# Kernel tuning notes

Measured on AMD Instinct MI355X. Metric: run time of the kernel, lower is better.

Reference implementation:

```python
import jax, jax.numpy as jnp
import numpy as np

B, S, DIM, EXTRA, NK, NH, NL = 16, 256, 41, 1, 128, 4, 3
ND = DIM + EXTRA  # 42 channels after appending the Time2Vec extra channel


def _lin(key, fin, fout):
    kw, kb = jax.random.split(key)
    w = jax.random.normal(kw, (fin, fout), jnp.float32) / np.float32(np.sqrt(fin))
    b = jax.random.normal(kb, (fout,), jnp.float32) * 0.01
    return w, b


def _stack(key, fin, fout):
    ws, bs = zip(*[_lin(k, fin, fout) for k in jax.random.split(key, NL)])
    return jnp.stack(ws), jnp.stack(bs)


def setup_inputs():
    key = jax.random.key(0)
    ks = jax.random.split(key, 32)
    inp = {}
    inp['context_x'] = jnp.sort(jax.random.uniform(ks[0], (B, S), jnp.float32), axis=1)
    inp['value'] = jax.random.normal(ks[1], (B, S, DIM), jnp.float32)
    mask = (jax.random.uniform(ks[2], (B, S, DIM)) < 0.23).astype(jnp.float32)
    inp['mask'] = mask
    inp['target_value'] = jax.random.normal(ks[3], (B, S, DIM), jnp.float32)
    inp['target_mask'] = mask * (jax.random.uniform(ks[4], (B, S, DIM)) < 0.3).astype(jnp.float32)
    inp['t2v_w0'] = jax.random.normal(ks[5], (1,), jnp.float32)
    inp['t2v_b0'] = jax.random.normal(ks[6], (1,), jnp.float32)
    inp['edge_w'], inp['edge_b'] = _lin(ks[7], 2, NK)
    inp['chan_w'], inp['chan_b'] = _lin(ks[8], ND, NK)
    inp['time_w'], inp['time_b'] = _lin(ks[9], 1, NK)
    base = 10
    for pre, dk in (('ct', 2 * NK), ('tc', 2 * NK), ('ca', NK)):
        inp[pre + '_wq'], inp[pre + '_bq'] = _stack(ks[base], NK, NK); base += 1
        inp[pre + '_wk'], inp[pre + '_bk'] = _stack(ks[base], dk, NK); base += 1
        inp[pre + '_wv'], inp[pre + '_bv'] = _stack(ks[base], dk, NK); base += 1
        inp[pre + '_wo'], inp[pre + '_bo'] = _stack(ks[base], NK, NK); base += 1
    inp['en_w'], inp['en_b'] = _stack(ks[base], 3 * NK, NK); base += 1
    inp['out_w'], inp['out_b'] = _lin(ks[base], 3 * NK, 1)
    return inp


def _mab2(Q, K, wq, bq, wk, bk, wv, bv, wo, bo, mask):
    # GraFITi MAB2: fc_q/fc_k/fc_v -> dim_out, multihead attn, O = Q + A@V, then O += relu(fc_o(O))
    q = Q @ wq + bq
    k = K @ wk + bk
    v = K @ wv + bv
    b, nq, d = q.shape
    dh = d // NH
    qh = q.reshape(b, nq, NH, dh)
    kh = k.reshape(b, -1, NH, dh)
    vh = v.reshape(b, -1, NH, dh)
    att = jnp.einsum('bqhd,bkhd->bhqk', qh, kh) / np.float32(np.sqrt(d))
    if mask is not None:
        att = jnp.where(mask[:, None] == 0, jnp.float32(-1e10), att)
    A = jax.nn.softmax(att, axis=-1)
    o = (qh + jnp.einsum('bhqk,bkhd->bqhd', A, vh)).reshape(b, nq, d)
    return o + jax.nn.relu(o @ wo + bo)


def _forward(context_x, value, mask, target_value, target_mask, t2v_w0, t2v_b0,
             edge_w, edge_b, chan_w, chan_b, time_w, time_b,
             ct_wq, ct_bq, ct_wk, ct_bk, ct_wv, ct_bv, ct_wo, ct_bo,
             tc_wq, tc_bq, tc_wk, tc_bk, tc_wv, tc_bv, tc_wo, tc_bo,
             en_w, en_b,
             ca_wq, ca_bq, ca_wk, ca_bk, ca_wv, ca_bv, ca_wo, ca_bo,
             out_w, out_b):
    te = (t2v_w0 * context_x + t2v_b0)[:, :, None]  # Time2Vec linear channel [B,S,1]
    value_f = jnp.concatenate([value, te], -1)  # [B,S,ND]
    mask_f = jnp.concatenate([mask, jnp.ones((B, S, EXTRA), jnp.float32)], -1)
    tval_f = jnp.concatenate([target_value, te], -1)
    tmask_f = jnp.concatenate([target_mask, jnp.zeros((B, S, EXTRA), jnp.float32)], -1)
    # ragged compaction: observed entries first, zero-padded to the batch max count
    full_len = int(np.asarray(jnp.max(jnp.sum(mask_f, axis=(1, 2)))))
    order = jnp.argsort(-mask_f.reshape(B, -1), axis=1, stable=True)[:, :full_len]
    take = lambda x: jnp.take_along_axis(x.reshape(B, -1), order, axis=1)
    mk_ = take(mask_f)  # [B,L]: ones then zero padding
    U_val = take(value_f) * mk_
    target_U_ = take(tval_f) * mk_
    target_mask_ = take(tmask_f) * mk_
    mki = mk_.astype(jnp.int32)
    T_inds_ = take(jnp.broadcast_to(jnp.arange(S, dtype=jnp.int32)[None, :, None], (B, S, ND))) * mki
    C_inds_ = take(jnp.broadcast_to(jnp.arange(ND, dtype=jnp.int32)[None, None, :], (B, S, ND))) * mki
    C_mask = (C_inds_[:, None, :] == jnp.arange(ND)[None, :, None]).astype(jnp.float32) * mk_[:, None, :]
    T_mask = (T_inds_[:, None, :] == jnp.arange(S)[None, :, None]).astype(jnp.float32) * mk_[:, None, :]
    U_ind = 1.0 - mk_ + target_mask_
    U = jax.nn.relu(jnp.stack([U_val, U_ind], -1) @ edge_w + edge_b) * mk_[:, :, None]  # [B,L,NK]
    T_ = jnp.sin(context_x[:, :, None] @ time_w + time_b)  # [B,S,NK]
    # one_hot(arange(ND)) @ chan_w == chan_w
    C_ = jnp.broadcast_to(jax.nn.relu(chan_w + chan_b)[None], (B, ND, NK))
    gT = lambda x, idx: jnp.take_along_axis(x, jnp.broadcast_to(idx[:, :, None], (B, full_len, NK)), axis=1)
    for i in range(NL):
        k_t = gT(T_, T_inds_)
        C2 = _mab2(C_, jnp.concatenate([k_t, U], -1), ct_wq[i], ct_bq[i], ct_wk[i], ct_bk[i], ct_wv[i], ct_bv[i], ct_wo[i], ct_bo[i], C_mask)
        k_c = gT(C_, C_inds_)
        T2 = _mab2(T_, jnp.concatenate([k_c, U], -1), tc_wq[i], tc_bq[i], tc_wk[i], tc_bk[i], tc_wv[i], tc_bv[i], tc_wo[i], tc_bo[i], T_mask)
        U = jax.nn.relu(U + jnp.concatenate([U, k_t, k_c], -1) @ en_w[i] + en_b[i]) * mk_[:, :, None]
        C_ = _mab2(C2, C2, ca_wq[i], ca_bq[i], ca_wk[i], ca_bk[i], ca_wv[i], ca_bv[i], ca_wo[i], ca_bo[i], None)
        T_ = T2
    k_t = gT(T_, T_inds_)
    k_c = gT(C_, C_inds_)
    output = jnp.concatenate([U, k_t, k_c], -1) @ out_w + out_b  # [B,L,1]
    return output, target_U_, target_mask_


def reference(context_x, value, mask, target_value, target_mask, t2v_w0, t2v_b0, edge_w, edge_b, chan_w, chan_b, time_w, time_b, ct_wq, ct_bq, ct_wk, ct_bk, ct_wv, ct_bv, ct_wo, ct_bo, tc_wq, tc_bq, tc_wk, tc_bk, tc_wv, tc_bv, tc_wo, tc_bo, en_w, en_b, ca_wq, ca_bq, ca_wk, ca_bk, ca_wv, ca_bv, ca_wo, ca_bo, out_w, out_b):
    return _forward(context_x, value, mask, target_value, target_mask, t2v_w0, t2v_b0, edge_w, edge_b, chan_w, chan_b, time_w, time_b, ct_wq, ct_bq, ct_wk, ct_bk, ct_wv, ct_bv, ct_wo, ct_bo, tc_wq, tc_bq, tc_wk, tc_bk, tc_wv, tc_bv, tc_wo, tc_bo, en_w, en_b, ca_wq, ca_bq, ca_wk, ca_bk, ca_wv, ca_bv, ca_wo, ca_bo, out_w, out_b)
```

## Files before the change

### kernel.cpp

```cpp
#include <hip/hip_runtime.h>
#include <math.h>

#define NB   16
#define SS   256
#define DIMV 41
#define NDV  42
#define NKD  128
#define NHD  4
#define DH   32
#define NLAY 3
#define TOT  (SS*NDV)
#define NCH  42

typedef __attribute__((ext_vector_type(8))) short short8;
typedef __attribute__((ext_vector_type(4))) float floatx4;

__device__ __forceinline__ short f2bf(float x) {
    unsigned u = __float_as_uint(x);
    u += 0x7fff + ((u >> 16) & 1);
    return (short)(u >> 16);
}
__device__ __forceinline__ float bfs2f(short s) {
    return __uint_as_float(((unsigned)(unsigned short)s) << 16);
}
__device__ __forceinline__ float bf2f(unsigned s) {
    return __uint_as_float(s << 16);
}

struct Seg { const short* ptr; const int* ind; int ns; };

__device__ __forceinline__ const short* seg_row(const Seg s, int gm, int Lb) {
    if (s.ind) {
        int b = gm / Lb;
        int id = s.ind[gm]; if (id < 0) id = 0;
        return s.ptr + ((size_t)b * s.ns + (size_t)id) * NKD;
    }
    return s.ptr + (size_t)gm * NKD;
}


__device__ __forceinline__ void compactA_body(int bx, const float* __restrict__ maskp,
                                              int* __restrict__ chunkcnt)
{
    const int b = bx / NCH, ch = bx % NCH;
    const int tid = threadIdx.x;
    const int idx = ch * 256 + tid;
    const int s = idx / NDV, c = idx % NDV;
    float m = (c < DIMV) ? maskp[((size_t)b*SS + s)*DIMV + c] : 1.0f;
    int x = (m != 0.0f) ? 1 : 0;
    #pragma unroll
    for (int off = 32; off; off >>= 1) x += __shfl_down(x, off);
    __shared__ int ws4[4];
    if ((tid & 63) == 0) ws4[tid >> 6] = x;
    __syncthreads();
    if (tid == 0) chunkcnt[bx] = ws4[0] + ws4[1] + ws4[2] + ws4[3];
}

__device__ __forceinline__ void zero_body(int bx, int* __restrict__ lo_t,
                                          int* __restrict__ hi_t)
{
    int i = bx*256 + threadIdx.x;
    if (i < NB*SS) { lo_t[i] = 0; hi_t[i] = 0; }
}

__device__ __forceinline__ void initT_body(int bx, const float* __restrict__ cx,
                                           const float* __restrict__ tw,
                                           const float* __restrict__ tb,
                                           short* __restrict__ T)
{
    int i = bx * 256 + threadIdx.x;
    if (i >= NB*SS*16) return;
    int row = i >> 4;
    int k = (i & 15) << 3;
    float t = cx[row];
    short8 r;
    #pragma unroll
    for (int j = 0; j < 8; j++) r[j] = f2bf(sinf(t*tw[k+j] + tb[k+j]));
    *(short8*)(T + (size_t)row*NKD + k) = r;
}

__device__ __forceinline__ void initC_body(int bx, const float* __restrict__ cw,
                                           const float* __restrict__ cb,
                                           short* __restrict__ C)
{
    int i = bx * 256 + threadIdx.x;
    if (i >= NB*NDV*16) return;
    int row = i >> 4;
    int c = row % NDV;
    int k = (i & 15) << 3;
    short8 r;
    #pragma unroll
    for (int j = 0; j < 8; j++) r[j] = f2bf(fmaxf(cw[(size_t)c*NKD + k+j] + cb[k+j], 0.f));
    *(short8*)(C + (size_t)row*NKD + k) = r;
}

template<int Kg>
__device__ __forceinline__ void prep1(const float* __restrict__ src,
                                      short* __restrict__ dst, int rel)
{
    const int per = Kg*128;
    int i = rel / per; int r2 = rel - i*per;
    int n = r2 / Kg;   int k = r2 - n*Kg;
    dst[rel] = f2bf(src[(size_t)i*per + (size_t)k*128 + n]);
}

#define W_TOTAL 933888
__device__ __forceinline__ void prepw_body(int bx,
    const float* ctq, const float* ctk, const float* ctv, const float* cto,
    const float* tcq, const float* tck, const float* tcv, const float* tco,
    const float* caq, const float* cak, const float* cav, const float* cao,
    const float* enw, short* __restrict__ arena)
{
    int idx = bx*256 + threadIdx.x;
    if (idx >= W_TOTAL) return;
    if      (idx < 49152 ) prep1<128>(ctq, arena + 0,      idx - 0);
    else if (idx < 147456) prep1<256>(ctk, arena + 49152,  idx - 49152);
    else if (idx < 245760) prep1<256>(ctv, arena + 147456, idx - 147456);
    else if (idx < 294912) prep1<128>(cto, arena + 245760, idx - 245760);
    else if (idx < 344064) prep1<128>(tcq, arena + 294912, idx - 294912);
    else if (idx < 442368) prep1<256>(tck, arena + 344064, idx - 344064);
    else if (idx < 540672) prep1<256>(tcv, arena + 442368, idx - 442368);
    else if (idx < 589824) prep1<128>(tco, arena + 540672, idx - 540672);
    else if (idx < 638976) prep1<128>(caq, arena + 589824, idx - 589824);
    else if (idx < 688128) prep1<128>(cak, arena + 638976, idx - 638976);
    else if (idx < 737280) prep1<128>(cav, arena + 688128, idx - 688128);
    else if (idx < 786432) prep1<128>(cao, arena + 737280, idx - 737280);
    else                   prep1<384>(enw, arena + 786432, idx - 786432);
}

__device__ __forceinline__ void trange_body(int bx, const int* __restrict__ tind,
                                            int* __restrict__ lo_t,
                                            int* __restrict__ hi_t, int L)
{
    int p = bx*256 + threadIdx.x;
    if (p >= NB*L) return;
    int b = p / L, l = p - b*L;
    int t = tind[p];
    if (t < 0) return;
    int tp = (l > 0) ? tind[p-1] : -999;
    int tn = (l+1 < L) ? tind[p+1] : -999;
    if (tp != t) lo_t[b*SS + t] = l;
    if (tn != t) hi_t[b*SS + t] = l+1;
}

__device__ __forceinline__ void cperm_body(int b, const int* __restrict__ cind,
                                           int* __restrict__ invp,
                                           int* __restrict__ clo,
                                           int* __restrict__ chi, int L)
{
    __shared__ int hist[NDV];
    __shared__ int base[NDV];
    __shared__ int padc, cntsh;
    const int tid = threadIdx.x;
    if (tid < NDV) hist[tid] = 0;
    if (tid == 0) padc = 0;
    __syncthreads();
    for (int l = tid; l < L; l += 256) {
        int c = cind[(size_t)b*L + l];
        if (c >= 0) atomicAdd(&hist[c], 1);
    }
    __syncthreads();
    if (tid == 0) {
        int run = 0;
        for (int c = 0; c < NDV; c++) {
            base[c] = run; clo[b*NDV + c] = run;
            run += hist[c]; chi[b*NDV + c] = run;
        }
        cntsh = run;
    }
    __syncthreads();
    if (tid < NDV) hist[tid] = 0;
    __syncthreads();
    const int cnt = cntsh;
    for (int l = tid; l < L; l += 256) {
        int c = cind[(size_t)b*L + l];
        int pos;
        if (c >= 0) pos = base[c] + atomicAdd(&hist[c], 1);
        else        pos = cnt + atomicAdd(&padc, 1);
        invp[(size_t)b*L + l] = b*L + pos;
    }
}

__device__ __forceinline__ void initU_body(int bx, const float* __restrict__ uval,
                                           const float* __restrict__ uind,
                                           const float* __restrict__ mkb,
                                           const float* __restrict__ ew,
                                           const float* __restrict__ eb,
                                           short* __restrict__ U, int BL)
{
    int i = bx * 256 + threadIdx.x;
    if (i >= BL*16) return;
    int row = i >> 4;
    int k = (i & 15) << 3;
    float uv = uval[row], ui = uind[row], m = mkb[row];
    short8 r;
    #pragma unroll
    for (int j = 0; j < 8; j++)
        r[j] = f2bf(fmaxf(uv*ew[k+j] + ui*ew[NKD+k+j] + eb[k+j], 0.f) * m);
    *(short8*)(U + (size_t)row*NKD + k) = r;
}

template<int NSEG, int MODE>
__device__ __forceinline__ void mgemm_body(char* smem, int bx,
           Seg s0, Seg s1, Seg s2, const short* __restrict__ Wt,
           const float* __restrict__ bias, short* __restrict__ D,
           int M, int Lb, const float* __restrict__ mkp)
{
    short (*As)[40] = (short (*)[40])smem;
    short (*Bs)[40] = (short (*)[40])(smem + 10240);
    const int bm = bx * 128;
    const int tid = threadIdx.x;
    const int wv = tid >> 6;
    const int lane = tid & 63;
    const int quad = lane >> 4;
    const int l16 = lane & 15;
    const int K = NSEG * 128;
    floatx4 acc[2][8];
    #pragma unroll
    for (int i = 0; i < 2; i++)
        #pragma unroll
        for (int j = 0; j < 8; j++) acc[i][j] = (floatx4){0.f,0.f,0.f,0.f};

    const int arow = tid >> 1;
    const int acol = (tid & 1) * 16;
    int gmc = bm + arow; if (gmc > M-1) gmc = M-1;
    const short* rowp0 = seg_row(s0, gmc, Lb);
    const short* rowp1 = (NSEG > 1) ? seg_row(s1, gmc, Lb) : nullptr;
    const short* rowp2 = (NSEG > 2) ? seg_row(s2, gmc, Lb) : nullptr;

    for (int k0 = 0; k0 < K; k0 += 32) {
        {
            const short* rp;
            if (NSEG == 1) rp = rowp0;
            else if (NSEG == 2) rp = (k0 < 128) ? rowp0 : rowp1;
            else rp = (k0 < 128) ? rowp0 : ((k0 < 256) ? rowp1 : rowp2);
            const int ks = k0 & 127;
            const short* src = rp + ks + acol;
            *(short8*)&As[arow][acol]   = *(const short8*)(src);
            *(short8*)&As[arow][acol+8] = *(const short8*)(src+8);
        }
        {
            const short* src = Wt + (size_t)arow*K + k0 + acol;
            *(short8*)&Bs[arow][acol]   = *(const short8*)(src);
            *(short8*)&Bs[arow][acol+8] = *(const short8*)(src+8);
        }
        __syncthreads();
        short8 af0 = *(short8*)&As[wv*32 + l16][quad*8];
        short8 af1 = *(short8*)&As[wv*32 + 16 + l16][quad*8];
        #pragma unroll
        for (int nf = 0; nf < 8; nf++) {
            short8 bf = *(short8*)&Bs[nf*16 + l16][quad*8];
            acc[0][nf] = __builtin_amdgcn_mfma_f32_16x16x32_bf16(af0, bf, acc[0][nf], 0, 0, 0);
            acc[1][nf] = __builtin_amdgcn_mfma_f32_16x16x32_bf16(af1, bf, acc[1][nf], 0, 0, 0);
        }
        __syncthreads();
    }
    #pragma unroll
    for (int mf = 0; mf < 2; mf++) {
        #pragma unroll
        for (int r = 0; r < 4; r++) {
            int gm = bm + wv*32 + mf*16 + quad*4 + r;
            if (gm < M) {
                float mk = (MODE == 3) ? mkp[gm] : 0.f;
                const short* res = (MODE == 2 || MODE == 3) ? seg_row(s0, gm, Lb) : nullptr;
                #pragma unroll
                for (int nf = 0; nf < 8; nf++) {
                    int gn = nf*16 + l16;
                    float val = acc[mf][nf][r] + bias[gn];
                    if (MODE == 2) val = bfs2f(res[gn]) + fmaxf(val, 0.f);
                    else if (MODE == 3) val = fmaxf(bfs2f(res[gn]) + val, 0.f) * mk;
                    D[(size_t)gm*NKD + gn] = f2bf(val);
                }
            }
        }
    }
}

template<int NSEG, bool HASQ>
__device__ __forceinline__ void mgemm_kv_body(char* smem, int bx,
              Seg s0, Seg s1,
              const short* __restrict__ Wk, const float* __restrict__ bk,
              const short* __restrict__ Wv, const float* __restrict__ bv,
              const short* __restrict__ Wq, const float* __restrict__ bq,
              short* __restrict__ Qd,
              unsigned* __restrict__ KV, int M, int Lb, const int* __restrict__ rmap)
{
    short (*As)[40] = (short (*)[40])smem;
    short (*Bk_)[40] = (short (*)[40])(smem + 5120);
    short (*Bv_)[40] = (short (*)[40])(smem + 15360);
    short (*Bq_)[40] = (short (*)[40])(smem + 25600);
    const int bm = bx * 64;
    const int tid = threadIdx.x;
    const int wv = tid >> 6;
    const int lane = tid & 63;
    const int quad = lane >> 4;
    const int l16 = lane & 15;
    const int K = NSEG * 128;
    floatx4 acck[8], accv[8], accq[8];
    #pragma unroll
    for (int j = 0; j < 8; j++) {
        acck[j] = (floatx4){0.f,0.f,0.f,0.f};
        accv[j] = (floatx4){0.f,0.f,0.f,0.f};
        if (HASQ) accq[j] = (floatx4){0.f,0.f,0.f,0.f};
    }

    const int arow = tid >> 2;
    const int acol = (tid & 3) * 8;
    const int brow = tid >> 1;
    const int bcol = (tid & 1) * 16;
    int gmc = bm + arow; if (gmc > M-1) gmc = M-1;
    const short* rowp0 = seg_row(s0, gmc, Lb);
    const short* rowp1 = (NSEG > 1) ? seg_row(s1, gmc, Lb) : nullptr;

    for (int k0 = 0; k0 < K; k0 += 32) {
        {
            const short* rp = (NSEG == 1) ? rowp0 : ((k0 < 128) ? rowp0 : rowp1);
            const int ks = k0 & 127;
            *(short8*)&As[arow][acol] = *(const short8*)(rp + ks + acol);
        }
        {
            const short* sk = Wk + (size_t)brow*K + k0 + bcol;
            *(short8*)&Bk_[brow][bcol]   = *(const short8*)(sk);
            *(short8*)&Bk_[brow][bcol+8] = *(const short8*)(sk+8);
            const short* sv = Wv + (size_t)brow*K + k0 + bcol;
            *(short8*)&Bv_[brow][bcol]   = *(const short8*)(sv);
            *(short8*)&Bv_[brow][bcol+8] = *(const short8*)(sv+8);
            if (HASQ) {
                const short* sq = Wq + (size_t)brow*K + k0 + bcol;
                *(short8*)&Bq_[brow][bcol]   = *(const short8*)(sq);
                *(short8*)&Bq_[brow][bcol+8] = *(const short8*)(sq+8);
            }
        }
        __syncthreads();
        short8 af = *(short8*)&As[wv*16 + l16][quad*8];
        #pragma unroll
        for (int nf = 0; nf < 8; nf++) {
            short8 bfk = *(short8*)&Bk_[nf*16 + l16][quad*8];
            acck[nf] = __builtin_amdgcn_mfma_f32_16x16x32_bf16(af, bfk, acck[nf], 0, 0, 0);
            short8 bfv = *(short8*)&Bv_[nf*16 + l16][quad*8];
            accv[nf] = __builtin_amdgcn_mfma_f32_16x16x32_bf16(af, bfv, accv[nf], 0, 0, 0);
            if (HASQ) {
                short8 bfq = *(short8*)&Bq_[nf*16 + l16][quad*8];
                accq[nf] = __builtin_amdgcn_mfma_f32_16x16x32_bf16(af, bfq, accq[nf], 0, 0, 0);
            }
        }
        __syncthreads();
    }
    #pragma unroll
    for (int r = 0; r < 4; r++) {
        int gm = bm + wv*16 + quad*4 + r;
        if (gm < M) {
            int orow = rmap ? rmap[gm] : gm;
            #pragma unroll
            for (int nf = 0; nf < 8; nf++) {
                int gn = nf*16 + l16;
                float kf = acck[nf][r] + bk[gn];
                float vf = accv[nf][r] + bv[gn];
                unsigned pk = (unsigned)(unsigned short)f2bf(kf)
                            | ((unsigned)(unsigned short)f2bf(vf) << 16);
                KV[(size_t)orow*NKD + gn] = pk;
                if (HASQ) Qd[(size_t)gm*NKD + gn] = f2bf(accq[nf][r] + bq[gn]);
            }
        }
    }
}

template<int SPLIT>
__device__ __forceinline__ void sattn_body(int bx,
                  const short* __restrict__ q, const unsigned* __restrict__ kvb,
                  short* __restrict__ o, int nq, int nkv,
                  const int* __restrict__ lo_arr, const int* __restrict__ hi_arr)
{
    __shared__ float sm_m[4], sm_s[4], sm_a[4][DH];
    const int wvid = threadIdx.x >> 6;
    int gtask = bx * 4 + wvid;
    int task = gtask / SPLIT;
    int part = gtask % SPLIT;
    if (task >= NB * nq * NHD) return;
    const int h = task & 3;
    const int bq = task >> 2;
    const int qi = bq % nq;
    const int b = bq / nq;
    const int lane = threadIdx.x & 63;
    const int d = lane & 31;
    const int half = lane >> 5;
    int lo = lo_arr ? lo_arr[b*nq + qi] : 0;
    int hi = hi_arr ? hi_arr[b*nq + qi] : nkv;
    if (SPLIT == 2) {
        int mid = lo + ((hi - lo + 1) >> 1);
        if (part == 0) hi = mid; else lo = mid;
    }
    const float scale = 0.088388347648318447f;

    const float qv = bfs2f(q[((size_t)(b*nq + qi))*NKD + h*DH + d]);
    const unsigned* kb = kvb + (size_t)b*nkv*NKD + h*DH + d;

    float m = -INFINITY, ssum = 0.f, acc = 0.f;
    for (int l0 = lo; l0 < hi; l0 += 8) {
        unsigned ur[4];
        #pragma unroll
        for (int j = 0; j < 4; j++) {
            int l = l0 + 2*j + half;
            bool ok = (l < hi);
            ur[j] = ok ? kb[(size_t)l*NKD] : 0u;
        }
        #pragma unroll
        for (int j = 0; j < 4; j++) {
            int l = l0 + 2*j + half;
            float kr = bf2f(ur[j] & 0xffffu);
            float vr = bf2f(ur[j] >> 16);
            float partial = qv * kr;
            #pragma unroll
            for (int off = 16; off; off >>= 1) partial += __shfl_xor(partial, off);
            float s = partial * scale;
            if (l < hi) {
                float mn = fmaxf(m, s);
                float corr = __expf(m - mn);
                float p = __expf(s - mn);
                ssum = ssum * corr + p;
                acc  = acc  * corr + p * vr;
                m = mn;
            }
        }
    }
    float mo = __shfl_xor(m, 32);
    float M = fmaxf(m, mo);
    float corr = (m > -1e30f) ? __expf(m - M) : 0.f;
    ssum *= corr; acc *= corr;
    ssum += __shfl_xor(ssum, 32);
    acc  += __shfl_xor(acc, 32);

    if (SPLIT == 1) {
        if (half == 0) {
            float res = (ssum > 0.f) ? acc / ssum : 0.f;
            o[((size_t)(b*nq + qi))*NKD + h*DH + d] = f2bf(qv + res);
        }
    } else {
        if (lane == 0) { sm_m[wvid] = M; sm_s[wvid] = ssum; }
        if (lane < DH) sm_a[wvid][lane] = acc;
        __syncthreads();
        if (part == 0 && lane < DH) {
            float m2 = sm_m[wvid+1], s2 = sm_s[wvid+1], a2 = sm_a[wvid+1][lane];
            float M2 = fmaxf(M, m2);
            float c1 = (M  > -1e30f) ? __expf(M  - M2) : 0.f;
            float c2 = (m2 > -1e30f) ? __expf(m2 - M2) : 0.f;
            float S = ssum * c1 + s2 * c2;
            float A = acc  * c1 + a2 * c2;
            float res = (S > 0.f) ? A / S : 0.f;
            float qv2 = bfs2f(q[((size_t)(b*nq + qi))*NKD + h*DH + lane]);
            o[((size_t)(b*nq + qi))*NKD + h*DH + lane] = f2bf(qv2 + res);
        }
    }
}


__global__ __launch_bounds__(256)
void k_pre1(const float* maskp, int* chunkcnt, int* lo_t, int* hi_t,
            const float* cx, const float* tw, const float* tb, short* T,
            const float* cw, const float* cb, short* C,
            const float* ctq, const float* ctk, const float* ctv, const float* cto,
            const float* tcq, const float* tck, const float* tcv, const float* tco,
            const float* caq, const float* cak, const float* cav, const float* cao,
            const float* enw, short* arena)
{
    int bx = blockIdx.x;
    if (bx < NB*NCH)            compactA_body(bx, maskp, chunkcnt);
    else if (bx < NB*NCH + 16)  zero_body(bx - NB*NCH, lo_t, hi_t);
    else if (bx < NB*NCH + 16 + 256) initT_body(bx - NB*NCH - 16, cx, tw, tb, T);
    else if (bx < NB*NCH + 16 + 256 + 42) initC_body(bx - NB*NCH - 16 - 256, cw, cb, C);
    else prepw_body(bx - NB*NCH - 16 - 256 - 42,
                    ctq, ctk, ctv, cto, tcq, tck, tcv, tco,
                    caq, cak, cav, cao, enw, arena);
}

__global__ __launch_bounds__(64)
void k_compactB(const int* __restrict__ chunkcnt, int* __restrict__ chunkoff,
                int* __restrict__ cntb)
{
    const int b = blockIdx.x, lane = threadIdx.x;
    int v = (lane < NCH) ? chunkcnt[b*NCH + lane] : 0;
    int x = v;
    #pragma unroll
    for (int off = 1; off < 64; off <<= 1) {
        int y = __shfl_up(x, off);
        if (lane >= off) x += y;
    }
    if (lane < NCH) chunkoff[b*NCH + lane] = x - v;
    if (lane == 63) cntb[b] = x;
}

__global__ __launch_bounds__(256)
void k_compactC(const float* __restrict__ cx, const float* __restrict__ value,
              const float* __restrict__ maskp, const float* __restrict__ tval,
              const float* __restrict__ tmaskp, const float* __restrict__ w0p,
              const float* __restrict__ b0p,
              const int* __restrict__ chunkoff, const int* __restrict__ cntb, int L,
              int* __restrict__ tind, int* __restrict__ cind,
              float* __restrict__ mkb, float* __restrict__ uval,
              float* __restrict__ uind,
              float* __restrict__ outTU, float* __restrict__ outTM)
{
    const int blk = blockIdx.x;
    const int b = blk / NCH, ch = blk % NCH;
    const int tid = threadIdx.x, lane = tid & 63, wv = tid >> 6;
    const int idx = ch * 256 + tid;
    const int s = idx / NDV, c = idx % NDV;
    float mval = (c < DIMV) ? maskp[((size_t)b*SS + s)*DIMV + c] : 1.0f;
    int m = (mval != 0.0f) ? 1 : 0;
    int x = m;
    #pragma unroll
    for (int off = 1; off < 64; off <<= 1) {
        int y = __shfl_up(x, off);
        if (lane >= off) x += y;
    }
    __shared__ int wsum[4];
    if (lane == 63) wsum[wv] = x;
    __syncthreads();
    int wbase = 0;
    for (int w = 0; w < wv; w++) wbase += wsum[w];
    const int excl = x - m + wbase;
    const int vbefore = chunkoff[b*NCH + ch] + excl;
    const int cnt = cntb[b];
    const int pos = m ? vbefore : (cnt + (idx - vbefore));
    if (pos < L) {
        const float w0 = w0p[0], b0 = b0p[0];
        float te = w0 * cx[(size_t)b*SS + s] + b0;
        float vf, tvf, tmf;
        if (c < DIMV) {
            size_t o = ((size_t)b*SS + s)*DIMV + c;
            vf = value[o]; tvf = tval[o]; tmf = tmaskp[o];
        } else { vf = te; tvf = te; tmf = 0.0f; }
        size_t p = (size_t)b*L + pos;
        if (m) {
            tind[p] = s; cind[p] = c; mkb[p] = 1.0f;
            uval[p] = vf; uind[p] = tmf;
            outTU[p] = tvf; outTM[p] = tmf;
        } else {
            tind[p] = -1; cind[p] = -1; mkb[p] = 0.0f;
            uval[p] = 0.0f; uind[p] = 1.0f;
            outTU[p] = 0.0f; outTM[p] = 0.0f;
        }
    }
}

__global__ __launch_bounds__(256)
void k_pre4(const int* tind, int* lo_t, int* hi_t, int L, int gTr,
            const int* cind, int* invp, int* clo, int* chi,
            const float* uval, const float* uind, const float* mkb,
            const float* ew, const float* eb, short* U, int BL)
{
    int bx = blockIdx.x;
    if (bx < gTr) trange_body(bx, tind, lo_t, hi_t, L);
    else if (bx < gTr + NB) cperm_body(bx - gTr, cind, invp, clo, chi, L);
    else initU_body(bx - gTr - NB, uval, uind, mkb, ew, eb, U, BL);
}

__global__ __launch_bounds__(256)
void k_phase1(int g0, int g1, int g2,
              const short* T1, const int* tind, const short* U,
              const short* wkct, const float* bkct, const short* wvct, const float* bvct,
              unsigned* KVct, const int* invp,
              const short* C1, const short* wqct, const float* bqct, short* qC,
              const int* cind,
              const short* wktc, const float* bktc, const short* wvtc, const float* bvtc,
              unsigned* KVtc,
              const short* wqtc, const float* bqtc, short* qT,
              int BL, int L)
{
    __shared__ __align__(16) char smem[25600];
    int bx = blockIdx.x;
    if (bx < g0) {
        mgemm_kv_body<2,false>(smem, bx, Seg{T1,tind,SS}, Seg{U,nullptr,0},
            wkct, bkct, wvct, bvct, nullptr, nullptr, nullptr, KVct, BL, L, invp);
    } else if (bx < g0+g1) {
        mgemm_body<1,0>(smem, bx-g0, Seg{C1,nullptr,0}, Seg{nullptr,nullptr,0},
            Seg{nullptr,nullptr,0}, wqct, bqct, qC, NB*NDV, 1, nullptr);
    } else if (bx < g0+g1+g2) {
        mgemm_kv_body<2,false>(smem, bx-g0-g1, Seg{C1,cind,NDV}, Seg{U,nullptr,0},
            wktc, bktc, wvtc, bvtc, nullptr, nullptr, nullptr, KVtc, BL, L, nullptr);
    } else {
        mgemm_body<1,0>(smem, bx-g0-g1-g2, Seg{T1,nullptr,0}, Seg{nullptr,nullptr,0},
            Seg{nullptr,nullptr,0}, wqtc, bqtc, qT, NB*SS, 1, nullptr);
    }
}

__global__ __launch_bounds__(256)
void k_phase2(int g0, const short* qC, const unsigned* KVct, short* oC,
              const int* clo, const int* chi, int L,
              const short* qT, const unsigned* KVtc, short* oT,
              const int* lo_t, const int* hi_t)
{
    int bx = blockIdx.x;
    if (bx < g0) sattn_body<2>(bx, qC, KVct, oC, NDV, L, clo, chi);
    else         sattn_body<1>(bx-g0, qT, KVtc, oT, SS, L, lo_t, hi_t);
}

__global__ __launch_bounds__(256)
void k_phase3(int g0, int g1,
              const short* oC, const short* woct, const float* boct, short* C2,
              const short* oT, const short* wotc, const float* botc, short* T2b,
              const short* U, const short* T1, const int* tind,
              const short* C1, const int* cind,
              const short* wen, const float* ben, short* Unew, const float* mkb,
              int BL, int L)
{
    __shared__ __align__(16) char smem[20480];
    int bx = blockIdx.x;
    if (bx < g0)
        mgemm_body<1,2>(smem, bx, Seg{oC,nullptr,0}, Seg{nullptr,nullptr,0},
            Seg{nullptr,nullptr,0}, woct, boct, C2, NB*NDV, 1, nullptr);
    else if (bx < g0+g1)
        mgemm_body<1,2>(smem, bx-g0, Seg{oT,nullptr,0}, Seg{nullptr,nullptr,0},
            Seg{nullptr,nullptr,0}, wotc, botc, T2b, NB*SS, 1, nullptr);
    else
        mgemm_body<3,3>(smem, bx-g0-g1, Seg{U,nullptr,0}, Seg{T1,tind,SS},
            Seg{C1,cind,NDV}, wen, ben, Unew, BL, L, mkb);
}

__global__ __launch_bounds__(256)
void k_ca_kvq(const short* C2, const short* wk, const float* bk,
              const short* wv, const float* bv, const short* wq, const float* bq,
              short* qC, unsigned* KV)
{
    __shared__ __align__(16) char smem[35840];
    mgemm_kv_body<1,true>(smem, blockIdx.x, Seg{C2,nullptr,0}, Seg{nullptr,nullptr,0},
                          wk, bk, wv, bv, wq, bq, qC, KV, NB*NDV, 1, nullptr);
}

__global__ __launch_bounds__(256)
void k_ca_attn(const short* qC, const unsigned* kv, short* oC)
{
    sattn_body<2>(blockIdx.x, qC, kv, oC, NDV, NDV, nullptr, nullptr);
}

__global__ __launch_bounds__(256)
void k_ca_oproj(const short* oC, const short* wo, const float* bo, short* C1)
{
    __shared__ __align__(16) char smem[20480];
    mgemm_body<1,2>(smem, blockIdx.x, Seg{oC,nullptr,0}, Seg{nullptr,nullptr,0},
                    Seg{nullptr,nullptr,0}, wo, bo, C1, NB*NDV, 1, nullptr);
}

__global__ __launch_bounds__(256)
void k_out(const short* __restrict__ U, const short* __restrict__ T1,
           const short* __restrict__ C1, const int* __restrict__ tind,
           const int* __restrict__ cind, const float* __restrict__ ow,
           const float* __restrict__ obp, float* __restrict__ out,
           int BL, int L)
{
    int row = blockIdx.x * 4 + (threadIdx.x >> 6);
    int lane = threadIdx.x & 63;
    if (row >= BL) return;
    int b = row / L;
    int ti = tind[row]; if (ti < 0) ti = 0;
    int ci = cind[row]; if (ci < 0) ci = 0;
    const short* u = U + (size_t)row*NKD;
    const short* a = T1 + ((size_t)(b*SS + ti))*NKD;
    const short* c = C1 + ((size_t)(b*NDV + ci))*NKD;
    float s = bfs2f(u[lane])*ow[lane]     + bfs2f(u[lane+64])*ow[lane+64]
            + bfs2f(a[lane])*ow[128+lane] + bfs2f(a[lane+64])*ow[192+lane]
            + bfs2f(c[lane])*ow[256+lane] + bfs2f(c[lane+64])*ow[320+lane];
    #pragma unroll
    for (int off = 32; off; off >>= 1) s += __shfl_down(s, off);
    if (lane == 0) out[row] = s + obp[0];
}

extern "C" void kernel_launch(void* const* d_in, const int* in_sizes, int n_in,
                              void* d_out, int out_size, void* d_ws, size_t ws_size,
                              hipStream_t stream)
{
    const float* cx     = (const float*)d_in[0];
    const float* value  = (const float*)d_in[1];
    const float* maskp  = (const float*)d_in[2];
    const float* tval   = (const float*)d_in[3];
    const float* tmaskp = (const float*)d_in[4];
    const float* w0     = (const float*)d_in[5];
    const float* b0     = (const float*)d_in[6];
    const float* edge_w = (const float*)d_in[7];
    const float* edge_b = (const float*)d_in[8];
    const float* chan_w = (const float*)d_in[9];
    const float* chan_b = (const float*)d_in[10];
    const float* time_w = (const float*)d_in[11];
    const float* time_b = (const float*)d_in[12];
    const float* ct_wq = (const float*)d_in[13];
    const float* ct_bq = (const float*)d_in[14];
    const float* ct_wk = (const float*)d_in[15];
    const float* ct_bk = (const float*)d_in[16];
    const float* ct_wv = (const float*)d_in[17];
    const float* ct_bv = (const float*)d_in[18];
    const float* ct_wo = (const float*)d_in[19];
    const float* ct_bo = (const float*)d_in[20];
    const float* tc_wq = (const float*)d_in[21];
    const float* tc_bq = (const float*)d_in[22];
    const float* tc_wk = (const float*)d_in[23];
    const float* tc_bk = (const float*)d_in[24];
    const float* tc_wv = (const float*)d_in[25];
    const float* tc_bv = (const float*)d_in[26];
    const float* tc_wo = (const float*)d_in[27];
    const float* tc_bo = (const float*)d_in[28];
    const float* ca_wq = (const float*)d_in[29];
    const float* ca_bq = (const float*)d_in[30];
    const float* ca_wk = (const float*)d_in[31];
    const float* ca_bk = (const float*)d_in[32];
    const float* ca_wv = (const float*)d_in[33];
    const float* ca_bv = (const float*)d_in[34];
    const float* ca_wo = (const float*)d_in[35];
    const float* ca_bo = (const float*)d_in[36];
    const float* en_w  = (const float*)d_in[37];
    const float* en_b  = (const float*)d_in[38];
    const float* out_w = (const float*)d_in[39];
    const float* out_b = (const float*)d_in[40];

    const int BL = out_size / 3;
    const int L  = BL / NB;

    char* p = (char*)d_ws;
    auto alloc = [&](size_t n) { char* r = p; p += (n + 255) & ~(size_t)255; return r; };
    int*      tind   = (int*)  alloc((size_t)BL*4);
    int*      cind   = (int*)  alloc((size_t)BL*4);
    float*    mkb    = (float*)alloc((size_t)BL*4);
    float*    uval   = (float*)alloc((size_t)BL*4);
    float*    uind   = (float*)alloc((size_t)BL*4);
    int*      lo_t   = (int*)  alloc((size_t)NB*SS*4);
    int*      hi_t   = (int*)  alloc((size_t)NB*SS*4);
    int*      clo    = (int*)  alloc((size_t)NB*NDV*4);
    int*      chi    = (int*)  alloc((size_t)NB*NDV*4);
    int*      invp   = (int*)  alloc((size_t)BL*4);
    int*      chunkc = (int*)  alloc((size_t)NB*NCH*4);
    int*      chunko = (int*)  alloc((size_t)NB*NCH*4);
    int*      cntb   = (int*)  alloc((size_t)NB*4);
    short*    waren  = (short*)alloc((size_t)W_TOTAL*2);
    short*    U    = (short*)alloc((size_t)BL*NKD*2);
    short*    Unew = (short*)alloc((size_t)BL*NKD*2);
    unsigned* KVct = (unsigned*)alloc((size_t)BL*NKD*4);
    unsigned* KVtc = (unsigned*)alloc((size_t)BL*NKD*4);
    unsigned* kvCa = (unsigned*)alloc((size_t)NB*NDV*NKD*4);
    short*    T1   = (short*)alloc((size_t)NB*SS*NKD*2);
    short*    T2b  = (short*)alloc((size_t)NB*SS*NKD*2);
    short*    qT   = (short*)alloc((size_t)NB*SS*NKD*2);
    short*    oT   = (short*)alloc((size_t)NB*SS*NKD*2);
    short*    C1   = (short*)alloc((size_t)NB*NDV*NKD*2);
    short*    C2   = (short*)alloc((size_t)NB*NDV*NKD*2);
    short*    qC   = (short*)alloc((size_t)NB*NDV*NKD*2);
    short*    oC   = (short*)alloc((size_t)NB*NDV*NKD*2);

    float* outMain = (float*)d_out;
    float* outTU = outMain + BL;
    float* outTM = outMain + 2*BL;

    const size_t OCTQ=0, OCTK=49152, OCTV=147456, OCTO=245760;
    const size_t OTCQ=294912, OTCK=344064, OTCV=442368, OTCO=540672;
    const size_t OCAQ=589824, OCAK=638976, OCAV=688128, OCAO=737280, OEN=786432;

    k_pre1<<<NB*NCH + 16 + 256 + 42 + W_TOTAL/256, 256, 0, stream>>>(
        maskp, chunkc, lo_t, hi_t, cx, time_w, time_b, T1, chan_w, chan_b, C1,
        ct_wq, ct_wk, ct_wv, ct_wo, tc_wq, tc_wk, tc_wv, tc_wo,
        ca_wq, ca_wk, ca_wv, ca_wo, en_w, waren);
    k_compactB<<<NB, 64, 0, stream>>>(chunkc, chunko, cntb);
    k_compactC<<<NB*NCH, 256, 0, stream>>>(cx, value, maskp, tval, tmaskp, w0, b0,
                                           chunko, cntb, L, tind, cind, mkb, uval, uind,
                                           outTU, outTM);
    {
        const int gTr = (NB*L + 255)/256;
        const int gU  = (BL*16 + 255)/256;
        k_pre4<<<gTr + NB + gU, 256, 0, stream>>>(
            tind, lo_t, hi_t, L, gTr, cind, invp, clo, chi,
            uval, uind, mkb, edge_w, edge_b, U, BL);
    }

    const int gBL  = (BL + 127)/128;
    const int gKV  = (BL + 63)/64;
    const int gC   = (NB*NDV + 127)/128;
    const int gT   = (NB*SS + 127)/128;
    const int gCa  = (NB*NDV + 63)/64;
    const int aC2  = NB*NDV*NHD*2/4;
    const int aTC  = NB*SS*NHD/4;

    for (int i = 0; i < NLAY; i++) {
        const size_t bOff = (size_t)i*NKD;
        const short* wq_ct = waren + OCTQ + (size_t)i*128*128;
        const short* wk_ct = waren + OCTK + (size_t)i*256*128;
        const short* wv_ct = waren + OCTV + (size_t)i*256*128;
        const short* wo_ct = waren + OCTO + (size_t)i*128*128;
        const short* wq_tc = waren + OTCQ + (size_t)i*128*128;
        const short* wk_tc = waren + OTCK + (size_t)i*256*128;
        const short* wv_tc = waren + OTCV + (size_t)i*256*128;
        const short* wo_tc = waren + OTCO + (size_t)i*128*128;
        const short* wq_ca = waren + OCAQ + (size_t)i*128*128;
        const short* wk_ca = waren + OCAK + (size_t)i*128*128;
        const short* wv_ca = waren + OCAV + (size_t)i*128*128;
        const short* wo_ca = waren + OCAO + (size_t)i*128*128;
        const short* w_en  = waren + OEN  + (size_t)i*384*128;

        k_phase1<<<gKV + gC + gKV + gT, 256, 0, stream>>>(
            gKV, gC, gKV,
            T1, tind, U,
            wk_ct, ct_bk + bOff, wv_ct, ct_bv + bOff, KVct, invp,
            C1, wq_ct, ct_bq + bOff, qC,
            cind, wk_tc, tc_bk + bOff, wv_tc, tc_bv + bOff, KVtc,
            wq_tc, tc_bq + bOff, qT, BL, L);
        k_phase2<<<aC2 + aTC, 256, 0, stream>>>(
            aC2, qC, KVct, oC, clo, chi, L, qT, KVtc, oT, lo_t, hi_t);
        k_phase3<<<gC + gT + gBL, 256, 0, stream>>>(
            gC, gT, oC, wo_ct, ct_bo + bOff, C2, oT, wo_tc, tc_bo + bOff, T2b,
            U, T1, tind, C1, cind, w_en, en_b + bOff, Unew, mkb, BL, L);
        k_ca_kvq<<<gCa, 256, 0, stream>>>(C2, wk_ca, ca_bk + bOff,
            wv_ca, ca_bv + bOff, wq_ca, ca_bq + bOff, qC, kvCa);
        k_ca_attn<<<aC2, 256, 0, stream>>>(qC, kvCa, oC);
        k_ca_oproj<<<gC, 256, 0, stream>>>(oC, wo_ca, ca_bo + bOff, C1);

        short* t = U;  U = Unew; Unew = t;
        t = T1; T1 = T2b; T2b = t;
    }

    k_out<<<(BL + 3)/4, 256, 0, stream>>>(U, T1, C1, tind, cind,
                                          out_w, out_b, outMain, BL, L);
}
```

Baseline: 468.2 us.

## Fuse channel self-attention into one per-batch kernel and inline compaction scan

Replaces the three channel-attention kernels (KVQ projection, attention, output projection) with one kernel. It runs one block per batch and keeps Q, K/V and the attention output in shared memory. Separately, the per-batch chunk prefix scan is folded into the compaction kernel, which removes a launch and its small offset buffers. This cuts launches and global round-trips per layer, but the fused kernel runs only 16 blocks and executes its projections serially, so it may leave much of the GPU idle.

```diff
diff --git a/kernel.cpp b/kernel.cpp
--- a/kernel.cpp
+++ b/kernel.cpp
@@ -276,19 +276,16 @@
     }
 }
 
-template<int NSEG, bool HASQ>
+template<int NSEG>
 __device__ __forceinline__ void mgemm_kv_body(char* smem, int bx,
               Seg s0, Seg s1,
               const short* __restrict__ Wk, const float* __restrict__ bk,
               const short* __restrict__ Wv, const float* __restrict__ bv,
-              const short* __restrict__ Wq, const float* __restrict__ bq,
-              short* __restrict__ Qd,
               unsigned* __restrict__ KV, int M, int Lb, const int* __restrict__ rmap)
 {
     short (*As)[40] = (short (*)[40])smem;
     short (*Bk_)[40] = (short (*)[40])(smem + 5120);
     short (*Bv_)[40] = (short (*)[40])(smem + 15360);
-    short (*Bq_)[40] = (short (*)[40])(smem + 25600);
     const int bm = bx * 64;
     const int tid = threadIdx.x;
     const int wv = tid >> 6;
@@ -296,12 +293,11 @@
     const int quad = lane >> 4;
     const int l16 = lane & 15;
     const int K = NSEG * 128;
-    floatx4 acck[8], accv[8], accq[8];
+    floatx4 acck[8], accv[8];
     #pragma unroll
     for (int j = 0; j < 8; j++) {
         acck[j] = (floatx4){0.f,0.f,0.f,0.f};
         accv[j] = (floatx4){0.f,0.f,0.f,0.f};
-        if (HASQ) accq[j] = (floatx4){0.f,0.f,0.f,0.f};
     }
 
     const int arow = tid >> 2;
@@ -325,11 +321,6 @@
             const short* sv = Wv + (size_t)brow*K + k0 + bcol;
             *(short8*)&Bv_[brow][bcol]   = *(const short8*)(sv);
             *(short8*)&Bv_[brow][bcol+8] = *(const short8*)(sv+8);
-            if (HASQ) {
-                const short* sq = Wq + (size_t)brow*K + k0 + bcol;
-                *(short8*)&Bq_[brow][bcol]   = *(const short8*)(sq);
-                *(short8*)&Bq_[brow][bcol+8] = *(const short8*)(sq+8);
-            }
         }
         __syncthreads();
         short8 af = *(short8*)&As[wv*16 + l16][quad*8];
@@ -339,10 +330,6 @@
             acck[nf] = __builtin_amdgcn_mfma_f32_16x16x32_bf16(af, bfk, acck[nf], 0, 0, 0);
             short8 bfv = *(short8*)&Bv_[nf*16 + l16][quad*8];
             accv[nf] = __builtin_amdgcn_mfma_f32_16x16x32_bf16(af, bfv, accv[nf], 0, 0, 0);
-            if (HASQ) {
-                short8 bfq = *(short8*)&Bq_[nf*16 + l16][quad*8];
-                accq[nf] = __builtin_amdgcn_mfma_f32_16x16x32_bf16(af, bfq, accq[nf], 0, 0, 0);
-            }
         }
         __syncthreads();
     }
@@ -359,7 +346,6 @@
                 unsigned pk = (unsigned)(unsigned short)f2bf(kf)
                             | ((unsigned)(unsigned short)f2bf(vf) << 16);
                 KV[(size_t)orow*NKD + gn] = pk;
-                if (HASQ) Qd[(size_t)gm*NKD + gn] = f2bf(accq[nf][r] + bq[gn]);
             }
         }
     }
@@ -473,28 +459,12 @@
                     caq, cak, cav, cao, enw, arena);
 }
 
-__global__ __launch_bounds__(64)
-void k_compactB(const int* __restrict__ chunkcnt, int* __restrict__ chunkoff,
-                int* __restrict__ cntb)
-{
-    const int b = blockIdx.x, lane = threadIdx.x;
-    int v = (lane < NCH) ? chunkcnt[b*NCH + lane] : 0;
-    int x = v;
-    #pragma unroll
-    for (int off = 1; off < 64; off <<= 1) {
-        int y = __shfl_up(x, off);
-        if (lane >= off) x += y;
-    }
-    if (lane < NCH) chunkoff[b*NCH + lane] = x - v;
-    if (lane == 63) cntb[b] = x;
-}
-
 __global__ __launch_bounds__(256)
 void k_compactC(const float* __restrict__ cx, const float* __restrict__ value,
               const float* __restrict__ maskp, const float* __restrict__ tval,
               const float* __restrict__ tmaskp, const float* __restrict__ w0p,
               const float* __restrict__ b0p,
-              const int* __restrict__ chunkoff, const int* __restrict__ cntb, int L,
+              const int* __restrict__ chunkcnt, int L,
               int* __restrict__ tind, int* __restrict__ cind,
               float* __restrict__ mkb, float* __restrict__ uval,
               float* __restrict__ uind,
@@ -514,13 +484,25 @@
         if (lane >= off) x += y;
     }
     __shared__ int wsum[4];
+    __shared__ int s_off, s_cnt;
     if (lane == 63) wsum[wv] = x;
+    if (tid < 64) {
+        int v2 = (tid < NCH) ? chunkcnt[b*NCH + tid] : 0;
+        int x2 = v2;
+        #pragma unroll
+        for (int off = 1; off < 64; off <<= 1) {
+            int y2 = __shfl_up(x2, off);
+            if (tid >= off) x2 += y2;
+        }
+        if (tid == ch) s_off = x2 - v2;
+        if (tid == 63) s_cnt = x2;
+    }
     __syncthreads();
     int wbase = 0;
     for (int w = 0; w < wv; w++) wbase += wsum[w];
     const int excl = x - m + wbase;
-    const int vbefore = chunkoff[b*NCH + ch] + excl;
-    const int cnt = cntb[b];
+    const int vbefore = s_off + excl;
+    const int cnt = s_cnt;
     const int pos = m ? vbefore : (cnt + (idx - vbefore));
     if (pos < L) {
         const float w0 = w0p[0], b0 = b0p[0];
@@ -570,14 +552,14 @@
     __shared__ __align__(16) char smem[25600];
     int bx = blockIdx.x;
     if (bx < g0) {
-        mgemm_kv_body<2,false>(smem, bx, Seg{T1,tind,SS}, Seg{U,nullptr,0},
-            wkct, bkct, wvct, bvct, nullptr, nullptr, nullptr, KVct, BL, L, invp);
+        mgemm_kv_body<2>(smem, bx, Seg{T1,tind,SS}, Seg{U,nullptr,0},
+            wkct, bkct, wvct, bvct, KVct, BL, L, invp);
     } else if (bx < g0+g1) {
         mgemm_body<1,0>(smem, bx-g0, Seg{C1,nullptr,0}, Seg{nullptr,nullptr,0},
             Seg{nullptr,nullptr,0}, wqct, bqct, qC, NB*NDV, 1, nullptr);
     } else if (bx < g0+g1+g2) {
-        mgemm_kv_body<2,false>(smem, bx-g0-g1, Seg{C1,cind,NDV}, Seg{U,nullptr,0},
-            wktc, bktc, wvtc, bvtc, nullptr, nullptr, nullptr, KVtc, BL, L, nullptr);
+        mgemm_kv_body<2>(smem, bx-g0-g1, Seg{C1,cind,NDV}, Seg{U,nullptr,0},
+            wktc, bktc, wvtc, bvtc, KVtc, BL, L, nullptr);
     } else {
         mgemm_body<1,0>(smem, bx-g0-g1-g2, Seg{T1,nullptr,0}, Seg{nullptr,nullptr,0},
             Seg{nullptr,nullptr,0}, wqtc, bqtc, qT, NB*SS, 1, nullptr);
@@ -618,27 +600,146 @@
 }
 
 __global__ __launch_bounds__(256)
-void k_ca_kvq(const short* C2, const short* wk, const float* bk,
-              const short* wv, const float* bv, const short* wq, const float* bq,
-              short* qC, unsigned* KV)
-{
-    __shared__ __align__(16) char smem[35840];
-    mgemm_kv_body<1,true>(smem, blockIdx.x, Seg{C2,nullptr,0}, Seg{nullptr,nullptr,0},
-                          wk, bk, wv, bv, wq, bq, qC, KV, NB*NDV, 1, nullptr);
-}
-
-__global__ __launch_bounds__(256)
-void k_ca_attn(const short* qC, const unsigned* kv, short* oC)
-{
-    sattn_body<2>(blockIdx.x, qC, kv, oC, NDV, NDV, nullptr, nullptr);
-}
-
-__global__ __launch_bounds__(256)
-void k_ca_oproj(const short* oC, const short* wo, const float* bo, short* C1)
-{
-    __shared__ __align__(16) char smem[20480];
-    mgemm_body<1,2>(smem, blockIdx.x, Seg{oC,nullptr,0}, Seg{nullptr,nullptr,0},
-                    Seg{nullptr,nullptr,0}, wo, bo, C1, NB*NDV, 1, nullptr);
+void k_caF(const short* __restrict__ C2,
+           const short* __restrict__ wk, const float* __restrict__ bk,
+           const short* __restrict__ wv, const float* __restrict__ bv,
+           const short* __restrict__ wq, const float* __restrict__ bq,
+           const short* __restrict__ wo, const float* __restrict__ bo,
+           short* __restrict__ C1)
+{
+    __shared__ short Xs[NDV][NKD];
+    __shared__ short Qs[NDV][NKD];
+    __shared__ unsigned KVs[NDV][NKD];
+    __shared__ short Os[NDV][NKD];
+    __shared__ short Bs[128][40];
+    const int b = blockIdx.x;
+    const int tid = threadIdx.x;
+    const int wvi = tid >> 6;
+    const int lane = tid & 63;
+    const int quad = lane >> 4;
+    const int l16 = lane & 15;
+    const int brow = tid >> 1;
+    const int bcol = (tid & 1) * 16;
+
+    for (int i = tid; i < NDV*16; i += 256) {
+        int row = i >> 4, col = (i & 15) << 3;
+        *(short8*)&Xs[row][col] = *(const short8*)(C2 + ((size_t)(b*NDV+row))*NKD + col);
+    }
+    __syncthreads();
+
+    floatx4 acck[8], accv[8], accq[8];
+    #pragma unroll
+    for (int j = 0; j < 8; j++) {
+        acck[j] = (floatx4){0,0,0,0}; accv[j] = (floatx4){0,0,0,0}; accq[j] = (floatx4){0,0,0,0};
+    }
+    int arow = wvi*16 + l16; if (arow >= NDV) arow = 0;
+    for (int proj = 0; proj < 3; proj++) {
+        const short* W = (proj == 0) ? wk : ((proj == 1) ? wv : wq);
+        for (int k0 = 0; k0 < 128; k0 += 32) {
+            __syncthreads();
+            const short* src = W + (size_t)brow*128 + k0 + bcol;
+            *(short8*)&Bs[brow][bcol]   = *(const short8*)(src);
+            *(short8*)&Bs[brow][bcol+8] = *(const short8*)(src+8);
+            __syncthreads();
+            short8 af = *(short8*)&Xs[arow][k0 + quad*8];
+            #pragma unroll
+            for (int nf = 0; nf < 8; nf++) {
+                short8 bf = *(short8*)&Bs[nf*16 + l16][quad*8];
+                if (proj == 0)      acck[nf] = __builtin_amdgcn_mfma_f32_16x16x32_bf16(af, bf, acck[nf], 0, 0, 0);
+                else if (proj == 1) accv[nf] = __builtin_amdgcn_mfma_f32_16x16x32_bf16(af, bf, accv[nf], 0, 0, 0);
+                else                accq[nf] = __builtin_amdgcn_mfma_f32_16x16x32_bf16(af, bf, accq[nf], 0, 0, 0);
+            }
+        }
+    }
+    __syncthreads();
+    #pragma unroll
+    for (int r = 0; r < 4; r++) {
+        int gm = wvi*16 + quad*4 + r;
+        if (gm < NDV) {
+            #pragma unroll
+            for (int nf = 0; nf < 8; nf++) {
+                int gn = nf*16 + l16;
+                float kf = acck[nf][r] + bk[gn];
+                float vf = accv[nf][r] + bv[gn];
+                KVs[gm][gn] = (unsigned)(unsigned short)f2bf(kf)
+                            | ((unsigned)(unsigned short)f2bf(vf) << 16);
+                Qs[gm][gn] = f2bf(accq[nf][r] + bq[gn]);
+            }
+        }
+    }
+    __syncthreads();
+
+    {
+        const float scale = 0.088388347648318447f;
+        const int d = lane & 31;
+        const int half = lane >> 5;
+        for (int task = wvi; task < NDV*NHD; task += 4) {
+            int qi = task >> 2;
+            int h = task & 3;
+            float qv = bfs2f(Qs[qi][h*DH + d]);
+            float m = -INFINITY, ssum = 0.f, acc = 0.f;
+            for (int l0 = 0; l0 < NDV; l0 += 2) {
+                int l = l0 + half;
+                bool ok = (l < NDV);
+                unsigned ur = ok ? KVs[l][h*DH + d] : 0u;
+                float kr = bf2f(ur & 0xffffu);
+                float vr = bf2f(ur >> 16);
+                float partial = qv * kr;
+                #pragma unroll
+                for (int off = 16; off; off >>= 1) partial += __shfl_xor(partial, off);
+                float s = partial * scale;
+                if (ok) {
+                    float mn = fmaxf(m, s);
+                    float corr = __expf(m - mn);
+                    float p = __expf(s - mn);
+                    ssum = ssum * corr + p;
+                    acc  = acc  * corr + p * vr;
+                    m = mn;
+                }
+            }
+            float mo = __shfl_xor(m, 32);
+            float M = fmaxf(m, mo);
+            float corr = (m > -1e30f) ? __expf(m - M) : 0.f;
+            ssum *= corr; acc *= corr;
+            ssum += __shfl_xor(ssum, 32);
+            acc  += __shfl_xor(acc, 32);
+            if (half == 0) {
+                float res = (ssum > 0.f) ? acc / ssum : 0.f;
+                Os[qi][h*DH + d] = f2bf(qv + res);
+            }
+        }
+    }
+    __syncthreads();
+
+    floatx4 acco[8];
+    #pragma unroll
+    for (int j = 0; j < 8; j++) acco[j] = (floatx4){0,0,0,0};
+    for (int k0 = 0; k0 < 128; k0 += 32) {
+        __syncthreads();
+        const short* src = wo + (size_t)brow*128 + k0 + bcol;
+        *(short8*)&Bs[brow][bcol]   = *(const short8*)(src);
+        *(short8*)&Bs[brow][bcol+8] = *(const short8*)(src+8);
+        __syncthreads();
+        short8 af = *(short8*)&Os[arow][k0 + quad*8];
+        #pragma unroll
+        for (int nf = 0; nf < 8; nf++) {
+            short8 bf = *(short8*)&Bs[nf*16 + l16][quad*8];
+            acco[nf] = __builtin_amdgcn_mfma_f32_16x16x32_bf16(af, bf, acco[nf], 0, 0, 0);
+        }
+    }
+    #pragma unroll
+    for (int r = 0; r < 4; r++) {
+        int gm = wvi*16 + quad*4 + r;
+        if (gm < NDV) {
+            #pragma unroll
+            for (int nf = 0; nf < 8; nf++) {
+                int gn = nf*16 + l16;
+                float val = acco[nf][r] + bo[gn];
+                val = bfs2f(Os[gm][gn]) + fmaxf(val, 0.f);
+                C1[((size_t)(b*NDV+gm))*NKD + gn] = f2bf(val);
+            }
+        }
+    }
 }
 
 __global__ __launch_bounds__(256)
@@ -727,14 +828,11 @@
     int*      chi    = (int*)  alloc((size_t)NB*NDV*4);
     int*      invp   = (int*)  alloc((size_t)BL*4);
     int*      chunkc = (int*)  alloc((size_t)NB*NCH*4);
-    int*      chunko = (int*)  alloc((size_t)NB*NCH*4);
-    int*      cntb   = (int*)  alloc((size_t)NB*4);
     short*    waren  = (short*)alloc((size_t)W_TOTAL*2);
     short*    U    = (short*)alloc((size_t)BL*NKD*2);
     short*    Unew = (short*)alloc((size_t)BL*NKD*2);
     unsigned* KVct = (unsigned*)alloc((size_t)BL*NKD*4);
     unsigned* KVtc = (unsigned*)alloc((size_t)BL*NKD*4);
-    unsigned* kvCa = (unsigned*)alloc((size_t)NB*NDV*NKD*4);
     short*    T1   = (short*)alloc((size_t)NB*SS*NKD*2);
     short*    T2b  = (short*)alloc((size_t)NB*SS*NKD*2);
     short*    qT   = (short*)alloc((size_t)NB*SS*NKD*2);
@@ -756,9 +854,8 @@
         maskp, chunkc, lo_t, hi_t, cx, time_w, time_b, T1, chan_w, chan_b, C1,
         ct_wq, ct_wk, ct_wv, ct_wo, tc_wq, tc_wk, tc_wv, tc_wo,
         ca_wq, ca_wk, ca_wv, ca_wo, en_w, waren);
-    k_compactB<<<NB, 64, 0, stream>>>(chunkc, chunko, cntb);
     k_compactC<<<NB*NCH, 256, 0, stream>>>(cx, value, maskp, tval, tmaskp, w0, b0,
-                                           chunko, cntb, L, tind, cind, mkb, uval, uind,
+                                           chunkc, L, tind, cind, mkb, uval, uind,
                                            outTU, outTM);
     {
         const int gTr = (NB*L + 255)/256;
@@ -772,7 +869,6 @@
     const int gKV  = (BL + 63)/64;
     const int gC   = (NB*NDV + 127)/128;
     const int gT   = (NB*SS + 127)/128;
-    const int gCa  = (NB*NDV + 63)/64;
     const int aC2  = NB*NDV*NHD*2/4;
     const int aTC  = NB*SS*NHD/4;
 
@@ -804,10 +900,9 @@
         k_phase3<<<gC + gT + gBL, 256, 0, stream>>>(
             gC, gT, oC, wo_ct, ct_bo + bOff, C2, oT, wo_tc, tc_bo + bOff, T2b,
             U, T1, tind, C1, cind, w_en, en_b + bOff, Unew, mkb, BL, L);
-        k_ca_kvq<<<gCa, 256, 0, stream>>>(C2, wk_ca, ca_bk + bOff,
-            wv_ca, ca_bv + bOff, wq_ca, ca_bq + bOff, qC, kvCa);
-        k_ca_attn<<<aC2, 256, 0, stream>>>(qC, kvCa, oC);
-        k_ca_oproj<<<gC, 256, 0, stream>>>(oC, wo_ca, ca_bo + bOff, C1);
+        k_caF<<<NB, 256, 0, stream>>>(C2,
+            wk_ca, ca_bk + bOff, wv_ca, ca_bv + bOff,
+            wq_ca, ca_bq + bOff, wo_ca, ca_bo + bOff, C1);
 
         short* t = U;  U = Unew; Unew = t;
         t = T1; T1 = T2b; T2b = t;
```

Measured after the change: 748.0 us. 1.6x slower.
